# Optimization experiments

Hardware: AMD Instinct MI355X
Metric: run time of the kernel (lower is better)

The kernel has to match this reference:

```python
import jax, jax.numpy as jnp
import numpy as np

IN_F = 128
OUT_F = 64
ALPHA = 0.2  # LeakyReLU negative slope


def setup_inputs() -> dict:
    key = jax.random.key(0)
    k1, k2, k3 = jax.random.split(key, 3)
    B, N = 8, 2048
    inp = jax.random.normal(k1, (B, N, IN_F), dtype=jnp.float32)
    adj = jnp.ones((B, N, N), dtype=jnp.float32)  # unused by the layer (no masking)
    # Parameters (xavier_uniform-style scale)
    w_lim = np.sqrt(6.0 / (IN_F + OUT_F))
    W = jax.random.uniform(k2, (OUT_F, IN_F), minval=-w_lim, maxval=w_lim, dtype=jnp.float32)
    a_lim = np.sqrt(6.0 / (2 * OUT_F + 1))
    a = jax.random.uniform(k3, (1, 2 * OUT_F), minval=-a_lim, maxval=a_lim, dtype=jnp.float32)
    return {"input": inp, "adj": adj, "W": W, "a": a}


def reference(input, adj, W, a):
    # h = W(input): [B, N, OUT_F]
    h = jnp.einsum("bnf,of->bno", input, W)
    # a^T [h_i || h_j] = a1^T h_i + a2^T h_j  (exact decomposition of the concat trick)
    a1 = a[0, :OUT_F]
    a2 = a[0, OUT_F:]
    s1 = jnp.einsum("bno,o->bn", h, a1)  # score contribution from node i
    s2 = jnp.einsum("bno,o->bn", h, a2)  # score contribution from node j
    e = s1[:, :, None] + s2[:, None, :]  # [B, N, N]
    e = jnp.where(e >= 0, e, ALPHA * e)  # LeakyReLU
    attention = jax.nn.softmax(e, axis=2)  # softmax over neighbors j (adj is NOT used)
    h_prime = jnp.einsum("bij,bjo->bio", attention, h)
    # concat=True -> ELU
    return jax.nn.elu(h_prime)
```

## Files before the change

kernel.cpp:

```cpp
#include <hip/hip_runtime.h>
#include <cstdio>

#define ALPHA 0.2f
constexpr int NN = 2048;
constexpr int NB = 8;
constexpr int FI = 128;
constexpr int FO = 64;
constexpr int SEG = 16;
constexpr int NSEG = NN / SEG;

__global__ __launch_bounds__(256) void k_h(const float* __restrict__ inp,
    const float* __restrict__ W, const float* __restrict__ a,
    float* __restrict__ h, float* __restrict__ s1, float* __restrict__ s2)
{
  __shared__ float4 Wq[(FI / 4) * FO];
  const int t = threadIdx.x;
  const float4* Wg = (const float4*)W;
#pragma unroll
  for (int i = 0; i < 8; ++i) {
    int f = t + i * 256;
    Wq[(f & 31) * FO + (f >> 5)] = Wg[f];
  }
  __syncthreads();
  const int lane = t & 63;
  const int wv = t >> 6;
  const size_t rowbase = ((size_t)blockIdx.x * 4 + wv) * 8;
  const float a1v = a[lane], a2v = a[FO + lane];
#pragma unroll
  for (int g = 0; g < 2; ++g) {
    const size_t r0 = rowbase + g * 4;
    const float4* x0 = (const float4*)(inp + r0 * FI);
    const float4* x1 = x0 + (FI / 4);
    const float4* x2 = x0 + 2 * (FI / 4);
    const float4* x3 = x0 + 3 * (FI / 4);
    float acc0 = 0.f, acc1 = 0.f, acc2 = 0.f, acc3 = 0.f;
#pragma unroll
    for (int cq = 0; cq < 32; ++cq) {
      float4 w = Wq[cq * FO + lane];
      float4 xa = x0[cq];
      acc0 = fmaf(xa.x, w.x, fmaf(xa.y, w.y, fmaf(xa.z, w.z, fmaf(xa.w, w.w, acc0))));
      float4 xb = x1[cq];
      acc1 = fmaf(xb.x, w.x, fmaf(xb.y, w.y, fmaf(xb.z, w.z, fmaf(xb.w, w.w, acc1))));
      float4 xc = x2[cq];
      acc2 = fmaf(xc.x, w.x, fmaf(xc.y, w.y, fmaf(xc.z, w.z, fmaf(xc.w, w.w, acc2))));
      float4 xd = x3[cq];
      acc3 = fmaf(xd.x, w.x, fmaf(xd.y, w.y, fmaf(xd.z, w.z, fmaf(xd.w, w.w, acc3))));
    }
    h[(r0 + 0) * FO + lane] = acc0;
    h[(r0 + 1) * FO + lane] = acc1;
    h[(r0 + 2) * FO + lane] = acc2;
    h[(r0 + 3) * FO + lane] = acc3;
    float p0 = acc0 * a1v, q0 = acc0 * a2v;
    float p1 = acc1 * a1v, q1 = acc1 * a2v;
    float p2 = acc2 * a1v, q2 = acc2 * a2v;
    float p3 = acc3 * a1v, q3 = acc3 * a2v;
#pragma unroll
    for (int off = 32; off; off >>= 1) {
      p0 += __shfl_down(p0, off); q0 += __shfl_down(q0, off);
      p1 += __shfl_down(p1, off); q1 += __shfl_down(q1, off);
      p2 += __shfl_down(p2, off); q2 += __shfl_down(q2, off);
      p3 += __shfl_down(p3, off); q3 += __shfl_down(q3, off);
    }
    if (lane == 0) {
      s1[r0 + 0] = p0; s2[r0 + 0] = q0;
      s1[r0 + 1] = p1; s2[r0 + 1] = q1;
      s1[r0 + 2] = p2; s2[r0 + 2] = q2;
      s1[r0 + 3] = p3; s2[r0 + 3] = q3;
    }
  }
}

__global__ __launch_bounds__(256) void k_count(
    const float* __restrict__ s1g, const float* __restrict__ s2g,
    int* __restrict__ sortedIdx, float* __restrict__ epS,
    float* __restrict__ eqS, int* __restrict__ kArr,
    float* __restrict__ zpArr, float* __restrict__ zqArr,
    float* __restrict__ m2g)
{
  __shared__ float sv[NN];
  __shared__ float s1l[NN];
  __shared__ float2 sepq[NN];
  __shared__ float red[256];
  __shared__ int   prk[64 * 4], pkk[64 * 4];
  __shared__ float pzp[64 * 4], pzq[64 * 4];
  const int b = blockIdx.x >> 5;
  const int c = blockIdx.x & 31;
  const int t = threadIdx.x;
  const int lane = t & 63;
  const int wv = t >> 6;
  for (int r = t; r < NN; r += 256) {
    sv[r] = s2g[b * NN + r];
    s1l[r] = s1g[b * NN + r];
  }
  __syncthreads();
  float mx = -1e30f;
#pragma unroll
  for (int i = 0; i < 8; ++i) mx = fmaxf(mx, sv[t + i * 256]);
  red[t] = mx;
  __syncthreads();
  for (int off = 128; off; off >>= 1) {
    if (t < off) red[t] = fmaxf(red[t], red[t + off]);
    __syncthreads();
  }
  const float m2 = red[0];
  if (c == 0 && t == 0) m2g[b] = m2;
#pragma unroll
  for (int rr = 0; rr < 8; ++rr) {
    const int i = t + rr * 256;
    const float v = sv[i];
    sepq[i] = make_float2(expf(v - m2), expf(ALPHA * (v - m2)));
  }
  __syncthreads();
  const int ib = c * 64 + lane;
  const float v = sv[ib];
  const float thr = -s1l[ib];
  int cR = 0, cK = 0;
  float zp = 0.f, zq = 0.f;
  const int j0 = wv * 512;
#pragma unroll 4
  for (int jj = 0; jj < 512; ++jj) {
    const int j = j0 + jj;
    const float x = sv[j];
    const float2 e = sepq[j];
    const bool pos = (x >= thr);
    cR += (x > v) || (x == v && j < ib);
    cK += pos;
    zp += pos ? e.x : 0.f;
    zq += pos ? 0.f : e.y;
  }
  prk[lane * 4 + wv] = cR;
  pkk[lane * 4 + wv] = cK;
  pzp[lane * 4 + wv] = zp;
  pzq[lane * 4 + wv] = zq;
  __syncthreads();
  if (t < 64) {
    int rank = 0, kk = 0;
    float zps = 0.f, zqs = 0.f;
#pragma unroll
    for (int i2 = 0; i2 < 4; ++i2) {
      rank += prk[t * 4 + i2]; kk += pkk[t * 4 + i2];
      zps += pzp[t * 4 + i2]; zqs += pzq[t * 4 + i2];
    }
    const int i = c * 64 + t;
    const float2 e = sepq[i];
    kArr[b * NN + i] = kk;
    zpArr[b * NN + i] = zps;
    zqArr[b * NN + i] = zqs;
    sortedIdx[b * NN + rank] = i;
    epS[b * NN + rank] = e.x;
    eqS[b * NN + rank] = e.y;
  }
}

__global__ __launch_bounds__(256) void k_seg(const float* __restrict__ h,
    const int* __restrict__ sortedIdx, const float* __restrict__ epS,
    const float* __restrict__ eqS,
    float* __restrict__ Lp, float* __restrict__ Lq,
    float* __restrict__ segTotP, float* __restrict__ segTotQ)
{
  const int lane = threadIdx.x & 63;
  const int s = blockIdx.x * 4 + (threadIdx.x >> 6);
  const int b = s >> 7;
  const int base = b * NN + (s & (NSEG - 1)) * SEG;
  float hv[SEG], wp[SEG], wq[SEG];
#pragma unroll
  for (int r = 0; r < SEG; ++r) {
    int idx = sortedIdx[base + r];
    hv[r] = h[((size_t)(b * NN + idx)) * FO + lane];
  }
#pragma unroll
  for (int r = 0; r < SEG; ++r) { wp[r] = epS[base + r]; wq[r] = eqS[base + r]; }
  float run = 0.f;
#pragma unroll
  for (int r = 0; r < SEG; ++r) {
    run = fmaf(wp[r], hv[r], run);
    Lp[(size_t)(base + r) * FO + lane] = run;
  }
  segTotP[(size_t)s * FO + lane] = run;
  run = 0.f;
#pragma unroll
  for (int r = SEG - 1; r >= 0; --r) {
    run = fmaf(wq[r], hv[r], run);
    Lq[(size_t)(base + r) * FO + lane] = run;
  }
  segTotQ[(size_t)s * FO + lane] = run;
}

__global__ __launch_bounds__(256) void k_out(const float* __restrict__ s1g,
    const int* __restrict__ kArr, const float* __restrict__ zpArr,
    const float* __restrict__ zqArr,
    const float* __restrict__ Lp, const float* __restrict__ Lq,
    const float* __restrict__ segTotP, const float* __restrict__ segTotQ,
    const float* __restrict__ m2g, float* __restrict__ out)
{
  __shared__ float cs[NSEG * FO];
  __shared__ float qt[4][FO];
  const int t = threadIdx.x;
  const int b = blockIdx.x >> 5;
  const int c = blockIdx.x & 31;
  const int lane = t & 63;
  const int wv = t >> 6;
  int kk[16];
#pragma unroll
  for (int rr = 0; rr < 16; ++rr)
    kk[rr] = kArr[b * NN + c * 64 + wv * 16 + rr];

  {
    const float4* sv4 = (const float4*)(segTotP + (size_t)b * NSEG * FO);
    float4* csv = (float4*)cs;
#pragma unroll
    for (int i = 0; i < NSEG * FO / 4 / 256; ++i) csv[t + i * 256] = sv4[t + i * 256];
  }
  __syncthreads();
  {
    float run = 0.f;
    for (int s = wv * 32; s < wv * 32 + 32; ++s) { run += cs[s * FO + lane]; cs[s * FO + lane] = run; }
    qt[wv][lane] = run;
  }
  __syncthreads();
  {
    float off = 0.f;
    for (int q2 = 0; q2 < wv; ++q2) off += qt[q2][lane];
    for (int s = wv * 32; s < wv * 32 + 32; ++s) cs[s * FO + lane] += off;
  }
  __syncthreads();
  float P[16];
#pragma unroll
  for (int rr = 0; rr < 16; ++rr) {
    const int k = kk[rr];
    P[rr] = 0.f;
    if (k > 0) {
      const int sP = (k - 1) >> 4;
      P[rr] = (sP > 0 ? cs[(sP - 1) * FO + lane] : 0.f) +
              Lp[((size_t)(b * NN + k - 1)) * FO + lane];
    }
  }
  __syncthreads();

  {
    const float4* sv4 = (const float4*)(segTotQ + (size_t)b * NSEG * FO);
    float4* csv = (float4*)cs;
#pragma unroll
    for (int i = 0; i < NSEG * FO / 4 / 256; ++i) csv[t + i * 256] = sv4[t + i * 256];
  }
  __syncthreads();
  {
    float run = 0.f;
    for (int s = wv * 32 + 31; s >= wv * 32; --s) { run += cs[s * FO + lane]; cs[s * FO + lane] = run; }
    qt[wv][lane] = run;
  }
  __syncthreads();
  {
    float off = 0.f;
    for (int q2 = wv + 1; q2 < 4; ++q2) off += qt[q2][lane];
    for (int s = wv * 32; s < wv * 32 + 32; ++s) cs[s * FO + lane] += off;
  }
  __syncthreads();
  float Q[16];
#pragma unroll
  for (int rr = 0; rr < 16; ++rr) {
    const int k = kk[rr];
    Q[rr] = 0.f;
    if (k < NN) {
      const int sQ = k >> 4;
      Q[rr] = (sQ < NSEG - 1 ? cs[(sQ + 1) * FO + lane] : 0.f) +
              Lq[((size_t)(b * NN + k)) * FO + lane];
    }
  }

  const float m2 = m2g[b];
#pragma unroll
  for (int rr = 0; rr < 16; ++rr) {
    const int i = c * 64 + wv * 16 + rr;
    const int gi = b * NN + i;
    const float u = s1g[gi] + m2;
    const float cmx = fmaxf(u, ALPHA * u);
    const float wp = expf(u - cmx);
    const float wq = expf(ALPHA * u - cmx);
    const float v = (wp * P[rr] + wq * Q[rr]) / (wp * zpArr[gi] + wq * zqArr[gi]);
    out[(size_t)gi * FO + lane] = (v > 0.f) ? v : expm1f(v);
  }
}

extern "C" void kernel_launch(void* const* d_in, const int* in_sizes, int n_in,
                              void* d_out, int out_size, void* d_ws, size_t ws_size,
                              hipStream_t stream) {
  const float* inp = (const float*)d_in[0];
  const float* W = (const float*)d_in[2];
  const float* a = (const float*)d_in[3];
  float* out = (float*)d_out;

  constexpr size_t NH = (size_t)NB * NN * FO;
  constexpr size_t NR = (size_t)NB * NN;
  constexpr size_t NST = (size_t)NB * NSEG * FO;
  constexpr size_t needFloats = 3 * NH + 8 * NR + 2 * NST + 8;
  if (ws_size < needFloats * sizeof(float)) {
    fprintf(stderr, "kernel_launch: ws too small (%zu < %zu)\n",
            ws_size, needFloats * sizeof(float));
    return;
  }
  float* ws = (float*)d_ws;
  float* h        = ws;
  float* Lp       = h + NH;
  float* Lq       = Lp + NH;
  float* s1       = Lq + NH;
  float* s2       = s1 + NR;
  int*   sortedIdx= (int*)(s2 + NR);
  float* epS      = (float*)(sortedIdx + NR);
  float* eqS      = epS + NR;
  int*   kArr     = (int*)(eqS + NR);
  float* zpArr    = (float*)(kArr + NR);
  float* zqArr    = zpArr + NR;
  float* segTotP  = zqArr + NR;
  float* segTotQ  = segTotP + NST;
  float* m2       = segTotQ + NST;

  k_h<<<512, 256, 0, stream>>>(inp, W, a, h, s1, s2);
  k_count<<<256, 256, 0, stream>>>(s1, s2, sortedIdx, epS, eqS,
                                   kArr, zpArr, zqArr, m2);
  k_seg<<<256, 256, 0, stream>>>(h, sortedIdx, epS, eqS, Lp, Lq,
                                 segTotP, segTotQ);
  k_out<<<256, 256, 0, stream>>>(s1, kArr, zpArr, zqArr, Lp, Lq,
                                 segTotP, segTotQ, m2, out);
}
```

Before: 79.81 us.

## Widen k_count to 512 threads with float4 LDS scans and shuffle max reduction

Doubles the k_count block to 512 threads, so each wave scans 256 neighbours instead of 512. The scan now reads the scores and the precomputed exponentials as float4 from separate LDS arrays and keeps split accumulators. The tree-based max reduction in shared memory becomes a wave shuffle plus a small per-wave array, and the per-block s1 staging is replaced by one direct global read. This cuts the serial inner-loop length and the barrier count in the ranking/partition-sum kernel, at the cost of more threads per block and a larger cross-wave partial reduction.

Result: faster. 69.57 us (-12.8%).

```diff
diff --git a/kernel.cpp b/kernel.cpp
--- a/kernel.cpp
+++ b/kernel.cpp
@@ -70,7 +70,7 @@
   }
 }
 
-__global__ __launch_bounds__(256) void k_count(
+__global__ __launch_bounds__(512) void k_count(
     const float* __restrict__ s1g, const float* __restrict__ s2g,
     int* __restrict__ sortedIdx, float* __restrict__ epS,
     float* __restrict__ eqS, int* __restrict__ kArr,
@@ -78,77 +78,83 @@
     float* __restrict__ m2g)
 {
   __shared__ float sv[NN];
-  __shared__ float s1l[NN];
-  __shared__ float2 sepq[NN];
-  __shared__ float red[256];
-  __shared__ int   prk[64 * 4], pkk[64 * 4];
-  __shared__ float pzp[64 * 4], pzq[64 * 4];
+  __shared__ float sepA[NN], seqA[NN];
+  __shared__ float wmx[8];
+  __shared__ int   prk[64 * 8], pkk[64 * 8];
+  __shared__ float pzp[64 * 8], pzq[64 * 8];
   const int b = blockIdx.x >> 5;
   const int c = blockIdx.x & 31;
   const int t = threadIdx.x;
   const int lane = t & 63;
   const int wv = t >> 6;
-  for (int r = t; r < NN; r += 256) {
-    sv[r] = s2g[b * NN + r];
-    s1l[r] = s1g[b * NN + r];
-  }
-  __syncthreads();
-  float mx = -1e30f;
-#pragma unroll
-  for (int i = 0; i < 8; ++i) mx = fmaxf(mx, sv[t + i * 256]);
-  red[t] = mx;
-  __syncthreads();
-  for (int off = 128; off; off >>= 1) {
-    if (t < off) red[t] = fmaxf(red[t], red[t + off]);
-    __syncthreads();
-  }
-  const float m2 = red[0];
+  float4* sv4 = (float4*)sv;
+  const float4* g4 = (const float4*)(s2g + (size_t)b * NN);
+  const float4 mine = g4[t];
+  sv4[t] = mine;
+  float mx = fmaxf(fmaxf(mine.x, mine.y), fmaxf(mine.z, mine.w));
+#pragma unroll
+  for (int off = 32; off; off >>= 1) mx = fmaxf(mx, __shfl_down(mx, off));
+  if (lane == 0) wmx[wv] = mx;
+  __syncthreads();
+  float m2 = wmx[0];
+#pragma unroll
+  for (int i = 1; i < 8; ++i) m2 = fmaxf(m2, wmx[i]);
   if (c == 0 && t == 0) m2g[b] = m2;
-#pragma unroll
-  for (int rr = 0; rr < 8; ++rr) {
-    const int i = t + rr * 256;
-    const float v = sv[i];
-    sepq[i] = make_float2(expf(v - m2), expf(ALPHA * (v - m2)));
+  {
+    float4 e1, e2;
+    e1.x = expf(mine.x - m2); e2.x = expf(ALPHA * (mine.x - m2));
+    e1.y = expf(mine.y - m2); e2.y = expf(ALPHA * (mine.y - m2));
+    e1.z = expf(mine.z - m2); e2.z = expf(ALPHA * (mine.z - m2));
+    e1.w = expf(mine.w - m2); e2.w = expf(ALPHA * (mine.w - m2));
+    ((float4*)sepA)[t] = e1;
+    ((float4*)seqA)[t] = e2;
   }
   __syncthreads();
   const int ib = c * 64 + lane;
   const float v = sv[ib];
-  const float thr = -s1l[ib];
-  int cR = 0, cK = 0;
-  float zp = 0.f, zq = 0.f;
-  const int j0 = wv * 512;
+  const float thr = -s1g[(size_t)b * NN + ib];
+  int cR0 = 0, cR1 = 0, cK0 = 0, cK1 = 0;
+  float zp0 = 0.f, zp1 = 0.f, zq0 = 0.f, zq1 = 0.f;
+  const float4* svv = (const float4*)sv;
+  const float4* epv = (const float4*)sepA;
+  const float4* eqv = (const float4*)seqA;
 #pragma unroll 4
-  for (int jj = 0; jj < 512; ++jj) {
-    const int j = j0 + jj;
-    const float x = sv[j];
-    const float2 e = sepq[j];
-    const bool pos = (x >= thr);
-    cR += (x > v) || (x == v && j < ib);
-    cK += pos;
-    zp += pos ? e.x : 0.f;
-    zq += pos ? 0.f : e.y;
-  }
-  prk[lane * 4 + wv] = cR;
-  pkk[lane * 4 + wv] = cK;
-  pzp[lane * 4 + wv] = zp;
-  pzq[lane * 4 + wv] = zq;
+  for (int j4 = wv * 64; j4 < wv * 64 + 64; ++j4) {
+    const float4 x = svv[j4];
+    const float4 e1 = epv[j4];
+    const float4 e2 = eqv[j4];
+    const int j = 4 * j4;
+    bool p0 = (x.x >= thr), p1 = (x.y >= thr), p2 = (x.z >= thr), p3 = (x.w >= thr);
+    cK0 += p0 + p1; cK1 += p2 + p3;
+    zp0 += (p0 ? e1.x : 0.f) + (p1 ? e1.y : 0.f);
+    zp1 += (p2 ? e1.z : 0.f) + (p3 ? e1.w : 0.f);
+    zq0 += (p0 ? 0.f : e2.x) + (p1 ? 0.f : e2.y);
+    zq1 += (p2 ? 0.f : e2.z) + (p3 ? 0.f : e2.w);
+    cR0 += ((x.x > v) || (x.x == v && (j + 0) < ib))
+         + ((x.y > v) || (x.y == v && (j + 1) < ib));
+    cR1 += ((x.z > v) || (x.z == v && (j + 2) < ib))
+         + ((x.w > v) || (x.w == v && (j + 3) < ib));
+  }
+  prk[lane * 8 + wv] = cR0 + cR1;
+  pkk[lane * 8 + wv] = cK0 + cK1;
+  pzp[lane * 8 + wv] = zp0 + zp1;
+  pzq[lane * 8 + wv] = zq0 + zq1;
   __syncthreads();
   if (t < 64) {
     int rank = 0, kk = 0;
     float zps = 0.f, zqs = 0.f;
 #pragma unroll
-    for (int i2 = 0; i2 < 4; ++i2) {
-      rank += prk[t * 4 + i2]; kk += pkk[t * 4 + i2];
-      zps += pzp[t * 4 + i2]; zqs += pzq[t * 4 + i2];
+    for (int i2 = 0; i2 < 8; ++i2) {
+      rank += prk[t * 8 + i2]; kk += pkk[t * 8 + i2];
+      zps += pzp[t * 8 + i2]; zqs += pzq[t * 8 + i2];
     }
     const int i = c * 64 + t;
-    const float2 e = sepq[i];
     kArr[b * NN + i] = kk;
     zpArr[b * NN + i] = zps;
     zqArr[b * NN + i] = zqs;
     sortedIdx[b * NN + rank] = i;
-    epS[b * NN + rank] = e.x;
-    eqS[b * NN + rank] = e.y;
+    epS[b * NN + rank] = sepA[i];
+    eqS[b * NN + rank] = seqA[i];
   }
 }
 
@@ -316,7 +322,7 @@
   float* m2       = segTotQ + NST;
 
   k_h<<<512, 256, 0, stream>>>(inp, W, a, h, s1, s2);
-  k_count<<<256, 256, 0, stream>>>(s1, s2, sortedIdx, epS, eqS,
+  k_count<<<256, 512, 0, stream>>>(s1, s2, sortedIdx, epS, eqS,
                                    kArr, zpArr, zqArr, m2);
   k_seg<<<256, 256, 0, stream>>>(h, sortedIdx, epS, eqS, Lp, Lq,
                                  segTotP, segTotQ);
```
